# Kernel optimization log

Measured on AMD Instinct MI355X. Metric: run time of the kernel, lower is better.

Reference implementation:

```python
import jax, jax.numpy as jnp
import numpy as np

N_CHARS, EMB, HID, SEQ = 256, 512, 2048, 4096

def setup_inputs() -> dict:
    key = jax.random.key(0)
    ks = jax.random.split(key, 13)
    s = lambda k, shape: jax.random.normal(k, shape, dtype=jnp.float32) * 0.02
    return {
        "input_seq": jax.random.randint(ks[0], (SEQ,), 0, N_CHARS, dtype=jnp.int32),
        "emb_table": s(ks[1], (N_CHARS, EMB)),
        "Wf": s(ks[2], (HID, EMB + HID)), "bf": s(ks[3], (HID,)),
        "Wi": s(ks[4], (HID, EMB + HID)), "bi": s(ks[5], (HID,)),
        "Wo": s(ks[6], (HID, EMB + HID)), "bo": s(ks[7], (HID,)),
        "Wc": s(ks[8], (HID, EMB + HID)), "bc": s(ks[9], (HID,)),
        "Wy": s(ks[10], (N_CHARS, HID)), "by": s(ks[11], (N_CHARS,)),
    }

def reference(input_seq, emb_table, Wf, bf, Wi, bi, Wo, bo, Wc, bc, Wy, by):
    E = emb_table.shape[1]
    embs = emb_table[input_seq]  # [T, E]
    # Split each gate Linear on concat([emb, h]) into input and recurrent parts.
    # Input contributions for all timesteps as one GEMM per gate: [T, H]
    xf = embs @ Wf[:, :E].T + bf
    xi = embs @ Wi[:, :E].T + bi
    xo = embs @ Wo[:, :E].T + bo
    xc = embs @ Wc[:, :E].T + bc
    Wfh, Wih, Woh, Wch = Wf[:, E:], Wi[:, E:], Wo[:, E:], Wc[:, E:]

    def step(carry, xs):
        h, c = carry
        xf_t, xi_t, xo_t, xc_t = xs
        ft = jax.nn.sigmoid(xf_t + Wfh @ h)
        it = jax.nn.sigmoid(xi_t + Wih @ h)
        tct = jnp.tanh(xc_t + Wch @ h)
        c_new = ft * c + it * tct
        ot = jax.nn.sigmoid(xo_t + Woh @ h)
        h_new = ot * jnp.tanh(c_new)
        o = Wy @ h_new + by
        return (h_new, c_new), o

    h0 = jnp.zeros((Wf.shape[0],), dtype=embs.dtype)
    c0 = jnp.zeros((Wf.shape[0],), dtype=embs.dtype)
    (h, c), outs = jax.lax.scan(step, (h0, c0), (xf, xi, xo, xc))
    return outs, h, c
```

## Files before the change

### kernel.cpp

```cpp
#include <hip/hip_runtime.h>
#include <hip/hip_fp16.h>

#define SEQL 4096
#define EMBD 512
#define HIDD 2048
#define NCH  256
#define WCOL 2560
#define NREP 8

typedef _Float16 half8_t  __attribute__((ext_vector_type(8)));
typedef _Float16 half2_t  __attribute__((ext_vector_type(2)));
typedef float    float4_t __attribute__((ext_vector_type(4)));
typedef unsigned uint4_t  __attribute__((ext_vector_type(4)));
typedef unsigned uint2_t  __attribute__((ext_vector_type(2)));

#if __has_builtin(__builtin_amdgcn_fdot2)
__device__ __forceinline__ float fdot2u(unsigned a, unsigned b, float c) {
  return __builtin_amdgcn_fdot2(__builtin_bit_cast(half2_t, a),
                                __builtin_bit_cast(half2_t, b), c, false);
}
#else
__device__ __forceinline__ float fdot2u(unsigned a, unsigned b, float c) {
  half2_t ha = __builtin_bit_cast(half2_t, a), hb = __builtin_bit_cast(half2_t, b);
  return c + (float)ha.x * (float)hb.x + (float)ha.y * (float)hb.y;
}
#endif

__device__ __forceinline__ float sigm_f(float x)  { return 1.f / (1.f + __expf(-x)); }
__device__ __forceinline__ float tanh_f(float x)  { return 1.f - 2.f / (__expf(2.f * x) + 1.f); }

__device__ __forceinline__ uint4_t poll_ld(const unsigned* p) {
  uint4_t r;
  asm volatile("global_load_dwordx4 %0, %1, off sc1\n\ts_waitcnt vmcnt(0)"
               : "=v"(r) : "v"(p) : "memory");
  return r;
}
__device__ __forceinline__ int ok4(uint4_t v, unsigned tg) {
  return ((v.x >> 16) == tg) & ((v.y >> 16) == tg) &
         ((v.z >> 16) == tg) & ((v.w >> 16) == tg);
}

__global__ void prep_kernel(const int* __restrict__ seq, const float* __restrict__ emb,
                            const float* __restrict__ Wf, const float* __restrict__ Wi,
                            const float* __restrict__ Wo, const float* __restrict__ Wc,
                            const float* __restrict__ Wy,
                            _Float16* __restrict__ emb16, _Float16* __restrict__ Wst16,
                            _Float16* __restrict__ Wy16, unsigned* __restrict__ hx)
{
  const long nEmb = (long)SEQL * EMBD;
  const long nWst = (long)4 * HIDD * EMBD;
  const long nWy  = (long)NCH * HIDD;
  const long nHx  = (long)NREP * 2 * HIDD;
  const long total = nEmb + nWst + nWy + nHx;
  long stride = (long)gridDim.x * blockDim.x;
  for (long i = (long)blockIdx.x * blockDim.x + threadIdx.x; i < total; i += stride) {
    if (i < nEmb) {
      long t = i >> 9, e = i & 511;
      emb16[i] = (_Float16)emb[(long)seq[t] * EMBD + e];
    } else if (i < nEmb + nWst) {
      long j = i - nEmb;
      long row = j >> 9, k = j & 511;
      long r = row >> 11, jr = row & 2047;
      const float* W = (r == 0) ? Wf : (r == 1) ? Wi : (r == 2) ? Wo : Wc;
      Wst16[j] = (_Float16)W[jr * WCOL + k];
    } else if (i < nEmb + nWst + nWy) {
      long j = i - nEmb - nWst;
      Wy16[j] = (_Float16)Wy[j];
    } else {
      hx[i - nEmb - nWst - nWy] = 0u;
    }
  }
}

template<int K, int MODE>
__global__ __launch_bounds__(256) void gemm_bt(const _Float16* __restrict__ A,
                                               const _Float16* __restrict__ B,
                                               _Float16* __restrict__ C16,
                                               float* __restrict__ Cf,
                                               const float* __restrict__ bias, int N)
{
  __shared__ _Float16 At[128 * 32];
  __shared__ _Float16 Bt[128 * 32];
  const int tid = threadIdx.x;
  const int w = tid >> 6, lane = tid & 63;
  const int wm = w >> 1, wn = w & 1;
  const int lr = lane & 15, kg = lane >> 4;
  const long tm = (long)blockIdx.y * 128;
  const long tn = (long)blockIdx.x * 128;

  float4_t acc[4][4];
#pragma unroll
  for (int a = 0; a < 4; a++)
#pragma unroll
    for (int b = 0; b < 4; b++) acc[a][b] = (float4_t)0.f;

  for (int kt = 0; kt < K; kt += 32) {
    __syncthreads();
#pragma unroll
    for (int s = 0; s < 2; s++) {
      int l = s * 256 + tid;
      int row = l >> 2, ks = (l & 3) * 8;
      *(uint4*)&At[row * 32 + ks] = *(const uint4*)&A[(tm + row) * (long)K + kt + ks];
      *(uint4*)&Bt[row * 32 + ks] = *(const uint4*)&B[(tn + row) * (long)K + kt + ks];
    }
    __syncthreads();
    half8_t af[4], bf[4];
#pragma unroll
    for (int mi = 0; mi < 4; mi++) af[mi] = *(const half8_t*)&At[(wm * 64 + mi * 16 + lr) * 32 + kg * 8];
#pragma unroll
    for (int ni = 0; ni < 4; ni++) bf[ni] = *(const half8_t*)&Bt[(wn * 64 + ni * 16 + lr) * 32 + kg * 8];
#pragma unroll
    for (int mi = 0; mi < 4; mi++)
#pragma unroll
      for (int ni = 0; ni < 4; ni++)
        acc[mi][ni] = __builtin_amdgcn_mfma_f32_16x16x32_f16(af[mi], bf[ni], acc[mi][ni], 0, 0, 0);
  }

#pragma unroll
  for (int mi = 0; mi < 4; mi++)
#pragma unroll
    for (int ni = 0; ni < 4; ni++)
#pragma unroll
      for (int i = 0; i < 4; i++) {
        long gm = tm + wm * 64 + mi * 16 + kg * 4 + i;
        long gn = tn + wn * 64 + ni * 16 + lr;
        float v = acc[mi][ni][i];
        if (MODE == 0) C16[gm * (long)N + gn] = (_Float16)v;
        else           Cf[gm * (long)N + gn] = v + bias[gn];
      }
}

__global__ __launch_bounds__(512) void lstm_seq(
    const _Float16* __restrict__ xq,
    const float* __restrict__ Wf, const float* __restrict__ Wi,
    const float* __restrict__ Wo, const float* __restrict__ Wc,
    const float* __restrict__ bfp, const float* __restrict__ bip,
    const float* __restrict__ bop, const float* __restrict__ bcp,
    unsigned* __restrict__ hx,
    _Float16* __restrict__ H16,
    float* __restrict__ out)
{
  __shared__ uint2_t hbuf2[2][512];

  const int tid  = threadIdx.x;
  const int w    = tid >> 6, lane = tid & 63;
  const int rw   = lane >> 4, hsub = lane & 15;
  const int g    = blockIdx.x;
  const int jg   = g * 8 + w;
  const int rep  = g & (NREP - 1);

  const float* Wsel = (rw == 0) ? Wf : (rw == 1) ? Wi : (rw == 2) ? Wo : Wc;
  const float* bsel = (rw == 0) ? bfp : (rw == 1) ? bip : (rw == 2) ? bop : bcp;
  const float* wrow = Wsel + (long)jg * WCOL + EMBD;

  uint2 wreg[32];
#pragma unroll
  for (int it = 0; it < 32; ++it) {
    const float4 wv = *(const float4*)(wrow + it * 64 + hsub * 4);
    half2_t lo = { (_Float16)wv.x, (_Float16)wv.y };
    half2_t hi = { (_Float16)wv.z, (_Float16)wv.w };
    wreg[it].x = __builtin_bit_cast(unsigned, lo);
    wreg[it].y = __builtin_bit_cast(unsigned, hi);
  }
  const float bias = (hsub == 0) ? bsel[jg] : 0.f;

  float c = 0.f;

  for (int t = 0; t < SEQL; ++t) {
    const int par = t & 1;
    float xv = 0.f;
    if (hsub == 0) xv = (float)xq[(long)t * 8192 + rw * HIDD + jg];

    if (t == 0) {
      uint2_t z; z.x = 0u; z.y = 0u;
      hbuf2[0][tid] = z;
    } else {
      const unsigned* slice = hx + ((long)rep * 2 + par) * HIDD + tid * 4;
      const unsigned tg = (unsigned)t;
      uint4_t v;
      int guard = 0;
      for (;;) {
        v = poll_ld(slice);
        if (ok4(v, tg)) break;
        if (++guard > (1 << 22)) break;
      }
      uint2_t p;
      p.x = (v.x & 0xffffu) | (v.y << 16);
      p.y = (v.z & 0xffffu) | (v.w << 16);
      hbuf2[par][tid] = p;
    }
    __syncthreads();

    float a0 = 0.f, a1 = 0.f, a2 = 0.f, a3 = 0.f;
#pragma unroll
    for (int it = 0; it < 32; ++it) {
      const uint2_t hv = hbuf2[par][it * 16 + hsub];
      if (it & 1) { a2 = fdot2u(wreg[it].x, hv.x, a2); a3 = fdot2u(wreg[it].y, hv.y, a3); }
      else        { a0 = fdot2u(wreg[it].x, hv.x, a0); a1 = fdot2u(wreg[it].y, hv.y, a1); }
    }
    float s = (a0 + a1) + (a2 + a3);
    s += __shfl_xor(s, 1, 64);
    s += __shfl_xor(s, 2, 64);
    s += __shfl_xor(s, 4, 64);
    s += __shfl_xor(s, 8, 64);

    float act = 0.f;
    if (hsub == 0) {
      const float pre = s + xv + bias;
      act = (rw == 3) ? tanh_f(pre) : sigm_f(pre);
    }
    const float af = __shfl(act, 0,  64);
    const float ai = __shfl(act, 16, 64);
    const float ao = __shfl(act, 32, 64);
    const float ac = __shfl(act, 48, 64);

    if (lane == 0) {
      c = af * c + ai * ac;
      const float h = ao * tanh_f(c);
      const _Float16 hh = (_Float16)h;
      const unsigned pk = (unsigned)__builtin_bit_cast(unsigned short, hh)
                        | ((unsigned)(t + 1) << 16);
      const long poff = (long)((t + 1) & 1) * HIDD + jg;
#pragma unroll
      for (int rp = 0; rp < NREP; ++rp)
        __hip_atomic_store(hx + (long)rp * 2 * HIDD + poff, pk,
                           __ATOMIC_RELAXED, __HIP_MEMORY_SCOPE_AGENT);
      H16[(long)t * HIDD + jg] = hh;
      if (t == SEQL - 1) {
        out[(long)SEQL * NCH + jg] = h;
        out[(long)SEQL * NCH + HIDD + jg] = c;
      }
    }
  }
}

extern "C" void kernel_launch(void* const* d_in, const int* in_sizes, int n_in,
                              void* d_out, int out_size, void* d_ws, size_t ws_size,
                              hipStream_t stream) {
  const int*   seq = (const int*)d_in[0];
  const float* emb = (const float*)d_in[1];
  const float* Wf  = (const float*)d_in[2];
  const float* bf_ = (const float*)d_in[3];
  const float* Wi  = (const float*)d_in[4];
  const float* bi_ = (const float*)d_in[5];
  const float* Wo  = (const float*)d_in[6];
  const float* bo_ = (const float*)d_in[7];
  const float* Wc  = (const float*)d_in[8];
  const float* bc_ = (const float*)d_in[9];
  const float* Wy  = (const float*)d_in[10];
  const float* by  = (const float*)d_in[11];
  float* out = (float*)d_out;

  char* ws = (char*)d_ws;
  _Float16* xq     = (_Float16*)(ws);
  _Float16* emb16  = (_Float16*)(ws + (64ll << 20));
  _Float16* Wst16  = (_Float16*)(ws + (68ll << 20));
  _Float16* Wy16   = (_Float16*)(ws + (76ll << 20));
  _Float16* H16    = (_Float16*)(ws + (77ll << 20));
  unsigned* hx     = (unsigned*)(ws + (93ll << 20));

  prep_kernel<<<2048, 256, 0, stream>>>(seq, emb, Wf, Wi, Wo, Wc, Wy,
                                        emb16, Wst16, Wy16, hx);

  dim3 g1(8192 / 128, 4096 / 128);
  gemm_bt<EMBD, 0><<<g1, 256, 0, stream>>>(emb16, Wst16, xq, nullptr, nullptr, 8192);

  lstm_seq<<<256, 512, 0, stream>>>(xq, Wf, Wi, Wo, Wc, bf_, bi_, bo_, bc_,
                                    hx, H16, out);

  dim3 g2(NCH / 128, 4096 / 128);
  gemm_bt<HIDD, 1><<<g2, 256, 0, stream>>>(H16, Wy16, nullptr, out, by, NCH);
}
```

Measured before the change: 8.796 ms.

## Replace per-step block barrier with per-wave LDS flags and drop hx replicas

Removes the 8-way replication of the hidden-state exchange buffer, so each producer does one atomic store per step instead of eight and all blocks poll one shared copy. Replaces the per-timestep __syncthreads with per-wave LDS flags, so each wave waits only for the two waves that filled the quarter of the h buffer it is about to consume. This lets the dot product start in pieces as data arrives. In exchange, the single copy puts more polling traffic on the same cache lines. The volatile spin loops on LDS flags also carry ordering and correctness risks, since there is no barrier protecting reuse of the double buffer.

```diff
diff --git a/kernel.cpp b/kernel.cpp
--- a/kernel.cpp
+++ b/kernel.cpp
@@ -6,7 +6,6 @@
 #define HIDD 2048
 #define NCH  256
 #define WCOL 2560
-#define NREP 8
 
 typedef _Float16 half8_t  __attribute__((ext_vector_type(8)));
 typedef _Float16 half2_t  __attribute__((ext_vector_type(2)));
@@ -50,7 +49,7 @@
   const long nEmb = (long)SEQL * EMBD;
   const long nWst = (long)4 * HIDD * EMBD;
   const long nWy  = (long)NCH * HIDD;
-  const long nHx  = (long)NREP * 2 * HIDD;
+  const long nHx  = 2 * HIDD;
   const long total = nEmb + nWst + nWy + nHx;
   long stride = (long)gridDim.x * blockDim.x;
   for (long i = (long)blockIdx.x * blockDim.x + threadIdx.x; i < total; i += stride) {
@@ -141,13 +140,15 @@
     float* __restrict__ out)
 {
   __shared__ uint2_t hbuf2[2][512];
+  __shared__ int flags[8];
 
   const int tid  = threadIdx.x;
   const int w    = tid >> 6, lane = tid & 63;
   const int rw   = lane >> 4, hsub = lane & 15;
   const int g    = blockIdx.x;
   const int jg   = g * 8 + w;
-  const int rep  = g & (NREP - 1);
+  const int pairp = w >> 1, half = w & 1;
+  const int di   = pairp * 128 + half * 64 + lane;
 
   const float* Wsel = (rw == 0) ? Wf : (rw == 1) ? Wi : (rw == 2) ? Wo : Wc;
   const float* bsel = (rw == 0) ? bfp : (rw == 1) ? bip : (rw == 2) ? bop : bcp;
@@ -164,6 +165,10 @@
   }
   const float bias = (hsub == 0) ? bsel[jg] : 0.f;
 
+  if (tid < 8) flags[tid] = -1;
+  __syncthreads();
+
+  volatile int* vf = flags;
   float c = 0.f;
 
   for (int t = 0; t < SEQL; ++t) {
@@ -173,9 +178,9 @@
 
     if (t == 0) {
       uint2_t z; z.x = 0u; z.y = 0u;
-      hbuf2[0][tid] = z;
+      hbuf2[0][di] = z;
     } else {
-      const unsigned* slice = hx + ((long)rep * 2 + par) * HIDD + tid * 4;
+      const unsigned* slice = hx + (long)par * HIDD + di * 4;
       const unsigned tg = (unsigned)t;
       uint4_t v;
       int guard = 0;
@@ -187,16 +192,25 @@
       uint2_t p;
       p.x = (v.x & 0xffffu) | (v.y << 16);
       p.y = (v.z & 0xffffu) | (v.w << 16);
-      hbuf2[par][tid] = p;
-    }
-    __syncthreads();
+      hbuf2[par][di] = p;
+    }
+    asm volatile("s_waitcnt lgkmcnt(0)" ::: "memory");
+    if (lane == 0) vf[w] = t;
 
     float a0 = 0.f, a1 = 0.f, a2 = 0.f, a3 = 0.f;
 #pragma unroll
-    for (int it = 0; it < 32; ++it) {
-      const uint2_t hv = hbuf2[par][it * 16 + hsub];
-      if (it & 1) { a2 = fdot2u(wreg[it].x, hv.x, a2); a3 = fdot2u(wreg[it].y, hv.y, a3); }
-      else        { a0 = fdot2u(wreg[it].x, hv.x, a0); a1 = fdot2u(wreg[it].y, hv.y, a1); }
+    for (int q = 0; q < 4; ++q) {
+      int guard2 = 0;
+      while (vf[2 * q] < t || vf[2 * q + 1] < t) {
+        if (++guard2 > (1 << 24)) break;
+      }
+#pragma unroll
+      for (int s5 = 0; s5 < 8; ++s5) {
+        const int it = q * 8 + s5;
+        const uint2_t hv = hbuf2[par][it * 16 + hsub];
+        if (it & 1) { a2 = fdot2u(wreg[it].x, hv.x, a2); a3 = fdot2u(wreg[it].y, hv.y, a3); }
+        else        { a0 = fdot2u(wreg[it].x, hv.x, a0); a1 = fdot2u(wreg[it].y, hv.y, a1); }
+      }
     }
     float s = (a0 + a1) + (a2 + a3);
     s += __shfl_xor(s, 1, 64);
@@ -220,11 +234,8 @@
       const _Float16 hh = (_Float16)h;
       const unsigned pk = (unsigned)__builtin_bit_cast(unsigned short, hh)
                         | ((unsigned)(t + 1) << 16);
-      const long poff = (long)((t + 1) & 1) * HIDD + jg;
-#pragma unroll
-      for (int rp = 0; rp < NREP; ++rp)
-        __hip_atomic_store(hx + (long)rp * 2 * HIDD + poff, pk,
-                           __ATOMIC_RELAXED, __HIP_MEMORY_SCOPE_AGENT);
+      __hip_atomic_store(hx + (long)((t + 1) & 1) * HIDD + jg, pk,
+                         __ATOMIC_RELAXED, __HIP_MEMORY_SCOPE_AGENT);
       H16[(long)t * HIDD + jg] = hh;
       if (t == SEQL - 1) {
         out[(long)SEQL * NCH + jg] = h;
```

Result: slower. 13.69 ms (+55.6%).

## Halve LSTM workgroups by computing two hidden units per wave, drop h replicas

Applied to the files above, without the earlier changes.

The persistent recurrent kernel now runs on 128 workgroups instead of 256. Each wave computes two hidden units, holding two weight rows in registers and reusing each LDS load of h for both dot products. The 8-way replicated h exchange buffer is replaced by a single copy, so each step issues fewer atomic stores and fewer workgroups spin-poll. In exchange, more workgroups poll the same global lines, and register use roughly doubles for weights, which may spill or limit occupancy.

```diff
diff --git a/kernel.cpp b/kernel.cpp
--- a/kernel.cpp
+++ b/kernel.cpp
@@ -6,7 +6,7 @@
 #define HIDD 2048
 #define NCH  256
 #define WCOL 2560
-#define NREP 8
+#define NWG  128
 
 typedef _Float16 half8_t  __attribute__((ext_vector_type(8)));
 typedef _Float16 half2_t  __attribute__((ext_vector_type(2)));
@@ -50,7 +50,7 @@
   const long nEmb = (long)SEQL * EMBD;
   const long nWst = (long)4 * HIDD * EMBD;
   const long nWy  = (long)NCH * HIDD;
-  const long nHx  = (long)NREP * 2 * HIDD;
+  const long nHx  = 2 * HIDD;
   const long total = nEmb + nWst + nWy + nHx;
   long stride = (long)gridDim.x * blockDim.x;
   for (long i = (long)blockIdx.x * blockDim.x + threadIdx.x; i < total; i += stride) {
@@ -146,36 +146,47 @@
   const int w    = tid >> 6, lane = tid & 63;
   const int rw   = lane >> 4, hsub = lane & 15;
   const int g    = blockIdx.x;
-  const int jg   = g * 8 + w;
-  const int rep  = g & (NREP - 1);
+  const int base = (g * 8 + w) * 2;
 
   const float* Wsel = (rw == 0) ? Wf : (rw == 1) ? Wi : (rw == 2) ? Wo : Wc;
   const float* bsel = (rw == 0) ? bfp : (rw == 1) ? bip : (rw == 2) ? bop : bcp;
-  const float* wrow = Wsel + (long)jg * WCOL + EMBD;
-
-  uint2 wreg[32];
+
+  uint2 wreg0[32], wreg1[32];
 #pragma unroll
   for (int it = 0; it < 32; ++it) {
-    const float4 wv = *(const float4*)(wrow + it * 64 + hsub * 4);
+    const float4 wv = *(const float4*)(Wsel + (long)base * WCOL + EMBD + it * 64 + hsub * 4);
     half2_t lo = { (_Float16)wv.x, (_Float16)wv.y };
     half2_t hi = { (_Float16)wv.z, (_Float16)wv.w };
-    wreg[it].x = __builtin_bit_cast(unsigned, lo);
-    wreg[it].y = __builtin_bit_cast(unsigned, hi);
-  }
-  const float bias = (hsub == 0) ? bsel[jg] : 0.f;
-
-  float c = 0.f;
+    wreg0[it].x = __builtin_bit_cast(unsigned, lo);
+    wreg0[it].y = __builtin_bit_cast(unsigned, hi);
+  }
+#pragma unroll
+  for (int it = 0; it < 32; ++it) {
+    const float4 wv = *(const float4*)(Wsel + (long)(base + 1) * WCOL + EMBD + it * 64 + hsub * 4);
+    half2_t lo = { (_Float16)wv.x, (_Float16)wv.y };
+    half2_t hi = { (_Float16)wv.z, (_Float16)wv.w };
+    wreg1[it].x = __builtin_bit_cast(unsigned, lo);
+    wreg1[it].y = __builtin_bit_cast(unsigned, hi);
+  }
+  const float b0 = (hsub == 0) ? bsel[base] : 0.f;
+  const float b1 = (hsub == 0) ? bsel[base + 1] : 0.f;
+
+  float c0 = 0.f, c1 = 0.f;
 
   for (int t = 0; t < SEQL; ++t) {
     const int par = t & 1;
-    float xv = 0.f;
-    if (hsub == 0) xv = (float)xq[(long)t * 8192 + rw * HIDD + jg];
+    float xv0 = 0.f, xv1 = 0.f;
+    if (hsub == 0) {
+      const unsigned xv2 = *(const unsigned*)(xq + (long)t * 8192 + rw * HIDD + base);
+      const half2_t xh = __builtin_bit_cast(half2_t, xv2);
+      xv0 = (float)xh.x; xv1 = (float)xh.y;
+    }
 
     if (t == 0) {
       uint2_t z; z.x = 0u; z.y = 0u;
       hbuf2[0][tid] = z;
     } else {
-      const unsigned* slice = hx + ((long)rep * 2 + par) * HIDD + tid * 4;
+      const unsigned* slice = hx + (long)par * HIDD + tid * 4;
       const unsigned tg = (unsigned)t;
       uint4_t v;
       int guard = 0;
@@ -191,44 +202,53 @@
     }
     __syncthreads();
 
-    float a0 = 0.f, a1 = 0.f, a2 = 0.f, a3 = 0.f;
+    float a00 = 0.f, a01 = 0.f, a10 = 0.f, a11 = 0.f;
 #pragma unroll
     for (int it = 0; it < 32; ++it) {
       const uint2_t hv = hbuf2[par][it * 16 + hsub];
-      if (it & 1) { a2 = fdot2u(wreg[it].x, hv.x, a2); a3 = fdot2u(wreg[it].y, hv.y, a3); }
-      else        { a0 = fdot2u(wreg[it].x, hv.x, a0); a1 = fdot2u(wreg[it].y, hv.y, a1); }
-    }
-    float s = (a0 + a1) + (a2 + a3);
-    s += __shfl_xor(s, 1, 64);
-    s += __shfl_xor(s, 2, 64);
-    s += __shfl_xor(s, 4, 64);
-    s += __shfl_xor(s, 8, 64);
-
-    float act = 0.f;
+      a00 = fdot2u(wreg0[it].x, hv.x, a00);
+      a01 = fdot2u(wreg0[it].y, hv.y, a01);
+      a10 = fdot2u(wreg1[it].x, hv.x, a10);
+      a11 = fdot2u(wreg1[it].y, hv.y, a11);
+    }
+    float s0 = a00 + a01, s1 = a10 + a11;
+    s0 += __shfl_xor(s0, 1, 64);  s1 += __shfl_xor(s1, 1, 64);
+    s0 += __shfl_xor(s0, 2, 64);  s1 += __shfl_xor(s1, 2, 64);
+    s0 += __shfl_xor(s0, 4, 64);  s1 += __shfl_xor(s1, 4, 64);
+    s0 += __shfl_xor(s0, 8, 64);  s1 += __shfl_xor(s1, 8, 64);
+
+    float act0 = 0.f, act1 = 0.f;
     if (hsub == 0) {
-      const float pre = s + xv + bias;
-      act = (rw == 3) ? tanh_f(pre) : sigm_f(pre);
-    }
-    const float af = __shfl(act, 0,  64);
-    const float ai = __shfl(act, 16, 64);
-    const float ao = __shfl(act, 32, 64);
-    const float ac = __shfl(act, 48, 64);
+      const float p0 = s0 + xv0 + b0;
+      const float p1 = s1 + xv1 + b1;
+      act0 = (rw == 3) ? tanh_f(p0) : sigm_f(p0);
+      act1 = (rw == 3) ? tanh_f(p1) : sigm_f(p1);
+    }
+    const float af0 = __shfl(act0, 0,  64), af1 = __shfl(act1, 0,  64);
+    const float ai0 = __shfl(act0, 16, 64), ai1 = __shfl(act1, 16, 64);
+    const float ao0 = __shfl(act0, 32, 64), ao1 = __shfl(act1, 32, 64);
+    const float ac0 = __shfl(act0, 48, 64), ac1 = __shfl(act1, 48, 64);
 
     if (lane == 0) {
-      c = af * c + ai * ac;
-      const float h = ao * tanh_f(c);
-      const _Float16 hh = (_Float16)h;
-      const unsigned pk = (unsigned)__builtin_bit_cast(unsigned short, hh)
-                        | ((unsigned)(t + 1) << 16);
-      const long poff = (long)((t + 1) & 1) * HIDD + jg;
-#pragma unroll
-      for (int rp = 0; rp < NREP; ++rp)
-        __hip_atomic_store(hx + (long)rp * 2 * HIDD + poff, pk,
-                           __ATOMIC_RELAXED, __HIP_MEMORY_SCOPE_AGENT);
-      H16[(long)t * HIDD + jg] = hh;
+      c0 = af0 * c0 + ai0 * ac0;
+      c1 = af1 * c1 + ai1 * ac1;
+      const float h0 = ao0 * tanh_f(c0);
+      const float h1 = ao1 * tanh_f(c1);
+      const _Float16 hh0 = (_Float16)h0, hh1 = (_Float16)h1;
+      const unsigned tag = (unsigned)(t + 1) << 16;
+      const unsigned pk0 = (unsigned)__builtin_bit_cast(unsigned short, hh0) | tag;
+      const unsigned pk1 = (unsigned)__builtin_bit_cast(unsigned short, hh1) | tag;
+      unsigned* dst = hx + (long)((t + 1) & 1) * HIDD + base;
+      __hip_atomic_store(dst,     pk0, __ATOMIC_RELAXED, __HIP_MEMORY_SCOPE_AGENT);
+      __hip_atomic_store(dst + 1, pk1, __ATOMIC_RELAXED, __HIP_MEMORY_SCOPE_AGENT);
+      const unsigned hpk = (unsigned)__builtin_bit_cast(unsigned short, hh0)
+                         | ((unsigned)__builtin_bit_cast(unsigned short, hh1) << 16);
+      *(unsigned*)&H16[(long)t * HIDD + base] = hpk;
       if (t == SEQL - 1) {
-        out[(long)SEQL * NCH + jg] = h;
-        out[(long)SEQL * NCH + HIDD + jg] = c;
+        out[(long)SEQL * NCH + base]            = h0;
+        out[(long)SEQL * NCH + base + 1]        = h1;
+        out[(long)SEQL * NCH + HIDD + base]     = c0;
+        out[(long)SEQL * NCH + HIDD + base + 1] = c1;
       }
     }
   }
@@ -265,7 +285,7 @@
   dim3 g1(8192 / 128, 4096 / 128);
   gemm_bt<EMBD, 0><<<g1, 256, 0, stream>>>(emb16, Wst16, xq, nullptr, nullptr, 8192);
 
-  lstm_seq<<<256, 512, 0, stream>>>(xq, Wf, Wi, Wo, Wc, bf_, bi_, bo_, bc_,
+  lstm_seq<<<NWG, 512, 0, stream>>>(xq, Wf, Wi, Wo, Wc, bf_, bi_, bo_, bc_,
                                     hx, H16, out);
 
   dim3 g2(NCH / 128, 4096 / 128);
```

Result: slower. 11.39 ms (+29.5%).
